# Kernel tuning notes

Measured on AMD Instinct MI355X. Metric: run time of the kernel, lower is better.

Reference implementation:

```python
import jax, jax.numpy as jnp
import numpy as np

V, C, D = 131072, 65536, 128
E_NEG, E_CON = 131072, 524288
L, B = 3, 32


def setup_inputs() -> dict:
    key = jax.random.key(0)
    ks = jax.random.split(key, 16)
    s = 1.0 / np.sqrt(D)
    return {
        "x_var": jax.random.normal(ks[0], (V, D), jnp.float32),
        "x_con": jax.random.normal(ks[1], (C, D), jnp.float32),
        "W_src": jax.random.normal(ks[2], (L, 3, D, D), jnp.float32) * s,
        "W_dst": jax.random.normal(ks[3], (L, 3, D, D), jnp.float32) * s,
        "att_src": jax.random.normal(ks[4], (L, 3, D), jnp.float32) * s,
        "att_dst": jax.random.normal(ks[5], (L, 3, D), jnp.float32) * s,
        "bias": jnp.zeros((L, 3, D), jnp.float32),
        "mlp_w1": jax.random.normal(ks[6], (D, D), jnp.float32) * s,
        "mlp_b1": jnp.zeros((D,), jnp.float32),
        "mlp_w2": jax.random.normal(ks[7], (D, 1), jnp.float32) * s,
        "mlp_b2": jnp.zeros((1,), jnp.float32),
        "edge_neg_src": jax.random.randint(ks[8], (E_NEG,), 0, V, jnp.int32),
        "edge_neg_dst": jax.random.randint(ks[9], (E_NEG,), 0, V, jnp.int32),
        "edge_con_src": jax.random.randint(ks[10], (E_CON,), 0, V, jnp.int32),
        "edge_con_dst": jax.random.randint(ks[11], (E_CON,), 0, C, jnp.int32),
        "batch_var": jnp.sort(jax.random.randint(ks[12], (V,), 0, B, jnp.int32)),
    }


def _gat(xs, xd, src, dst, Ws, Wd, a_s, a_d, b, n_dst):
    """PyG GATConv (heads=1, add_self_loops=False) for one bipartite relation."""
    hs = xs @ Ws                                    # [Ns, D]
    hd = xd @ Wd                                    # [Nd, D]
    es = hs @ a_s                                   # [Ns]
    ed = hd @ a_d                                   # [Nd]
    e = jax.nn.leaky_relu(es[src] + ed[dst], negative_slope=0.2)  # [E]
    m = jax.ops.segment_max(e, dst, num_segments=n_dst)
    m = jnp.where(jnp.isfinite(m), m, 0.0)
    ex = jnp.exp(e - m[dst])
    den = jax.ops.segment_sum(ex, dst, num_segments=n_dst)
    alpha = ex / (den[dst] + 1e-16)                 # per-destination softmax
    out = jax.ops.segment_sum(hs[src] * alpha[:, None], dst, num_segments=n_dst)
    return out + b


def reference(x_var, x_con, W_src, W_dst, att_src, att_dst, bias,
              mlp_w1, mlp_b1, mlp_w2, mlp_b2,
              edge_neg_src, edge_neg_dst, edge_con_src, edge_con_dst, batch_var):
    xv, xc = x_var, x_con
    n_layers = W_src.shape[0]
    for l in range(n_layers):
        # relation 0: variable -is_negation_of-> variable
        v_neg = _gat(xv, xv, edge_neg_src, edge_neg_dst,
                     W_src[l, 0], W_dst[l, 0], att_src[l, 0], att_dst[l, 0], bias[l, 0], V)
        # relation 2: constraint -rev_connected_to-> variable (reverse edges)
        v_rev = _gat(xc, xv, edge_con_dst, edge_con_src,
                     W_src[l, 2], W_dst[l, 2], att_src[l, 2], att_dst[l, 2], bias[l, 2], V)
        # relation 1: variable -connected_to-> constraint
        c_new = _gat(xv, xc, edge_con_src, edge_con_dst,
                     W_src[l, 1], W_dst[l, 1], att_src[l, 1], att_dst[l, 1], bias[l, 1], C)
        # HeteroConv aggr='sum', then relu (dropout is identity in eval)
        xv = jax.nn.relu(v_neg + v_rev)
        xc = jax.nn.relu(c_new)
    # global_mean_pool over variable nodes per graph
    cnt = jax.ops.segment_sum(jnp.ones((V,), xv.dtype), batch_var, num_segments=B)
    pooled = jax.ops.segment_sum(xv, batch_var, num_segments=B) / jnp.maximum(cnt, 1.0)[:, None]
    # vote MLP: Linear -> relu -> Linear
    h = jax.nn.relu(pooled @ mlp_w1 + mlp_b1)
    return h @ mlp_w2 + mlp_b2
```

## Files before the change

### kernel.cpp

```cpp
#include <hip/hip_runtime.h>
#include <hip/hip_bf16.h>
#include <cstdint>
#include <cstddef>

#define D 128

typedef __hip_bfloat16 bf16;
typedef __attribute__((ext_vector_type(8))) short short8v;
typedef __attribute__((ext_vector_type(4))) float f32x4;

__device__ inline float ld1(const float* p) { return *p; }
__device__ inline float ld1(const bf16* p) { return __bfloat162float(*p); }
__device__ inline float2 ld2(const float* p) { return *(const float2*)p; }
__device__ inline float2 ld2(const bf16* p) {
  __hip_bfloat162 v = *(const __hip_bfloat162*)p;
  float2 r; r.x = __bfloat162float(v.x); r.y = __bfloat162float(v.y); return r;
}
__device__ inline void st2(float* p, float a, float b) {
  float2 v; v.x = a; v.y = b; *(float2*)p = v;
}
__device__ inline void st2(bf16* p, float a, float b) {
  __hip_bfloat162 v; v.x = __float2bfloat16(a); v.y = __float2bfloat16(b);
  *(__hip_bfloat162*)p = v;
}

__device__ inline short f2bf(float x) {
  uint32_t u = __builtin_bit_cast(uint32_t, x);
  uint32_t r = (u + 0x7FFFu + ((u >> 16) & 1u)) >> 16;
  return (short)(uint16_t)r;
}
__device__ inline float bf2f(short s) {
  uint32_t u = ((uint32_t)(uint16_t)s) << 16;
  return __builtin_bit_cast(float, u);
}

__device__ inline f32x4 mfma16(short8v a, short8v b, f32x4 c) {
  return __builtin_amdgcn_mfma_f32_16x16x32_bf16(a, b, c, 0, 0, 0);
}

__device__ __forceinline__ void load8(const float* p, float* v) {
  float4 a = *(const float4*)p;
  float4 b = *(const float4*)(p + 4);
  v[0] = a.x; v[1] = a.y; v[2] = a.z; v[3] = a.w;
  v[4] = b.x; v[5] = b.y; v[6] = b.z; v[7] = b.w;
}
__device__ __forceinline__ void load8(const bf16* p, float* v) {
  short8v s = *(const short8v*)p;
  #pragma unroll
  for (int j = 0; j < 8; ++j) v[j] = bf2f(s[j]);
}
__device__ __forceinline__ void split_store(short* Xh, short* Xl, int off, const float* v) {
  short8v h, l;
  #pragma unroll
  for (int j = 0; j < 8; ++j) {
    short hj = f2bf(v[j]);
    h[j] = hj;
    l[j] = f2bf(v[j] - bf2f(hj));
  }
  *(short8v*)&Xh[off] = h;
  *(short8v*)&Xl[off] = l;
}

__global__ void compute_u_kernel(const float* __restrict__ Wsrc, const float* __restrict__ Wdst,
                                 const float* __restrict__ asrc, const float* __restrict__ adst,
                                 float* __restrict__ u) {
  int lr = blockIdx.x;
  int side = blockIdx.y;
  int k = threadIdx.x;
  const float* W = (side == 0 ? Wsrc : Wdst) + ((size_t)lr * D + k) * D;
  const float* a = (side == 0 ? asrc : adst) + (size_t)lr * D;
  float s = 0.f;
  for (int j = 0; j < D; ++j) s += W[j] * a[j];
  u[((size_t)lr * 2 + side) * D + k] = s;
}

__global__ void wsplit_kernel(const float* __restrict__ Wsrc,
                              short* __restrict__ WhT, short* __restrict__ WlT) {
  int lr = blockIdx.x;
  const float* W = Wsrc + (size_t)lr * D * D;
  short* wh = WhT + (size_t)lr * D * D;
  short* wl = WlT + (size_t)lr * D * D;
  for (int i = threadIdx.x; i < D * D; i += blockDim.x) {
    int k = i >> 7, c = i & 127;
    float w = W[i];
    short h = f2bf(w);
    short l = f2bf(w - bf2f(h));
    wh[c * D + k] = h;
    wl[c * D + k] = l;
  }
}

__global__ void count_kernel(const int* __restrict__ dst, int* __restrict__ cnt, int E) {
  int i = blockIdx.x * blockDim.x + threadIdx.x;
  if (i < E) atomicAdd(&cnt[dst[i]], 1);
}

__global__ void count2_kernel(const int* __restrict__ csrc, const int* __restrict__ cdst,
                              int* __restrict__ cnt_bycon, int* __restrict__ cnt_byvar, int E) {
  int i = blockIdx.x * blockDim.x + threadIdx.x;
  if (i < E) {
    atomicAdd(&cnt_bycon[cdst[i]], 1);
    atomicAdd(&cnt_byvar[csrc[i]], 1);
  }
}

__global__ void bsum3_kernel(const int* __restrict__ c0, const int* __restrict__ c1,
                             const int* __restrict__ c2, int* __restrict__ bsums,
                             int n0, int n1, int n2, int pb0, int pb1, int pb2) {
  __shared__ int red[256];
  int y = blockIdx.y;
  const int* cnt = (y == 0) ? c0 : (y == 1) ? c1 : c2;
  int n  = (y == 0) ? n0 : (y == 1) ? n1 : n2;
  int pb = (y == 0) ? pb0 : (y == 1) ? pb1 : pb2;
  int b = blockIdx.x, t = threadIdx.x;
  int base = b * pb;
  if (base >= n) return;
  int end = base + pb; if (end > n) end = n;
  int s = 0;
  for (int i = base + t; i < end; i += 256) s += cnt[i];
  red[t] = s;
  __syncthreads();
  #pragma unroll
  for (int off = 128; off; off >>= 1) {
    if (t < off) red[t] += red[t + off];
    __syncthreads();
  }
  if (t == 0) bsums[y * 1024 + b] = red[0];
}

__global__ void bscan3_kernel(int* __restrict__ bsums,
                              int* __restrict__ t0, int* __restrict__ t1, int* __restrict__ t2) {
  __shared__ int sh[1024];
  int y = blockIdx.x, t = threadIdx.x;
  int* bs = bsums + y * 1024;
  int v = bs[t];
  sh[t] = v;
  __syncthreads();
  for (int off = 1; off < 1024; off <<= 1) {
    int u = (t >= off) ? sh[t - off] : 0;
    __syncthreads();
    sh[t] += u;
    __syncthreads();
  }
  bs[t] = sh[t] - v;
  if (t == 1023) {
    int* tot = (y == 0) ? t0 : (y == 1) ? t1 : t2;
    *tot = sh[1023];
  }
}

__global__ void scanfill3_kernel(const int* __restrict__ c0, const int* __restrict__ c1,
                                 const int* __restrict__ c2, const int* __restrict__ bsums,
                                 int* __restrict__ rp0, int* __restrict__ rp1, int* __restrict__ rp2,
                                 int* __restrict__ cu0, int* __restrict__ cu1, int* __restrict__ cu2,
                                 int n0, int n1, int n2, int pb0, int pb1, int pb2) {
  __shared__ int sh[256];
  int y = blockIdx.y;
  const int* cnt = (y == 0) ? c0 : (y == 1) ? c1 : c2;
  int* rowptr    = (y == 0) ? rp0 : (y == 1) ? rp1 : rp2;
  int* cursor    = (y == 0) ? cu0 : (y == 1) ? cu1 : cu2;
  int n  = (y == 0) ? n0 : (y == 1) ? n1 : n2;
  int pb = (y == 0) ? pb0 : (y == 1) ? pb1 : pb2;
  int b = blockIdx.x, t = threadIdx.x;
  int base = b * pb;
  if (base >= n) return;
  int end = base + pb; if (end > n) end = n;
  int run = bsums[y * 1024 + b];
  for (int tile = base; tile < end; tile += 256) {
    int i = tile + t;
    int c = (i < end) ? cnt[i] : 0;
    __syncthreads();
    sh[t] = c;
    __syncthreads();
    for (int off = 1; off < 256; off <<= 1) {
      int u = (t >= off) ? sh[t - off] : 0;
      __syncthreads();
      sh[t] += u;
      __syncthreads();
    }
    int excl = sh[t] - c;
    if (i < end) {
      rowptr[i] = run + excl;
      cursor[i] = run + excl;
    }
    run += sh[255];
  }
}

__global__ void fill_kernel(const int* __restrict__ dst, const int* __restrict__ src,
                            int* __restrict__ cursor, int* __restrict__ col, int E) {
  int i = blockIdx.x * blockDim.x + threadIdx.x;
  if (i < E) {
    int p = atomicAdd(&cursor[dst[i]], 1);
    col[p] = src[i];
  }
}

__global__ void fill2_kernel(const int* __restrict__ csrc, const int* __restrict__ cdst,
                             int* __restrict__ cur_bycon, int* __restrict__ cur_byvar,
                             int* __restrict__ col_bycon, int* __restrict__ col_byvar, int E) {
  int i = blockIdx.x * blockDim.x + threadIdx.x;
  if (i < E) {
    int s = csrc[i], d = cdst[i];
    int p = atomicAdd(&cur_bycon[d], 1);
    col_bycon[p] = s;
    int q = atomicAdd(&cur_byvar[s], 1);
    col_byvar[q] = d;
  }
}

template<typename Tin>
__global__ __launch_bounds__(512) void mmv3_kernel(
    const Tin* __restrict__ Xv, const Tin* __restrict__ Xc,
    const short* __restrict__ wh0, const short* __restrict__ wl0,
    const short* __restrict__ wh1, const short* __restrict__ wl1,
    const short* __restrict__ wh2, const short* __restrict__ wl2,
    bf16* __restrict__ H0, bf16* __restrict__ H1, bf16* __restrict__ H2,
    const float* __restrict__ uv0, const float* __restrict__ uv1,
    const float* __restrict__ uv2, const float* __restrict__ uv3,
    const float* __restrict__ uc0, const float* __restrict__ uc1,
    float* __restrict__ es0, float* __restrict__ ed0,
    float* __restrict__ es1, float* __restrict__ ed2,
    float* __restrict__ es2, float* __restrict__ ed1,
    int V, int C, int b0, int b1, int b2) {
  __shared__ short sbuf[2][2][32 * 136];
  int bid = blockIdx.x;
  const Tin* X; const short* wh; const short* wl; bf16* H;
  int nrows, lb, nblk, ndots;
  const float *U0, *U1, *U2, *U3;
  float *O0, *O1, *O2, *O3;
  if (bid < b0) {
    X = Xv; wh = wh0; wl = wl0; H = H0; nrows = V; lb = bid; nblk = b0;
    ndots = 4; U0 = uv0; U1 = uv1; U2 = uv2; U3 = uv3;
    O0 = es0; O1 = ed0; O2 = es1; O3 = ed2;
  } else if (bid < b1) {
    X = Xv; wh = wh1; wl = wl1; H = H1; nrows = V; lb = bid - b0; nblk = b1 - b0;
    ndots = 0; U0 = U1 = U2 = U3 = nullptr; O0 = O1 = O2 = O3 = nullptr;
  } else {
    X = Xc; wh = wh2; wl = wl2; H = H2; nrows = C; lb = bid - b1; nblk = b2 - b1;
    ndots = 2; U0 = uc0; U1 = uc1; U2 = U3 = nullptr;
    O0 = es2; O1 = ed1; O2 = O3 = nullptr;
  }
  int nchunks = nrows >> 5;
  if (lb >= nchunks) return;

  int tid = threadIdx.x;
  int wv = tid >> 6, lane = tid & 63;
  int c15 = lane & 15, q = lane >> 4;
  int rowgrp = wv >> 2, colgrp = wv & 3;

  short8v Bh[2][4], Bl[2][4];
  #pragma unroll
  for (int t = 0; t < 2; ++t) {
    #pragma unroll
    for (int ks = 0; ks < 4; ++ks) {
      int o = (colgrp * 32 + t * 16 + c15) * D + ks * 32 + q * 8;
      Bh[t][ks] = *(const short8v*)&wh[o];
      Bl[t][ks] = *(const short8v*)&wl[o];
    }
  }

  int srow = tid >> 4;
  int scol = (tid & 15) * 8;
  int soff = srow * 136 + scol;

  float u0r[8], u1r[8], u2r[8], u3r[8];
  if (ndots) {
    load8(U0 + scol, u0r);
    load8(U1 + scol, u1r);
    if (ndots == 4) { load8(U2 + scol, u2r); load8(U3 + scol, u3r); }
  }

  auto do_dots = [&](const float* v, int gr) {
    if (!ndots) return;
    float p0 = 0.f, p1 = 0.f, p2 = 0.f, p3 = 0.f;
    #pragma unroll
    for (int j = 0; j < 8; ++j) { p0 += v[j] * u0r[j]; p1 += v[j] * u1r[j]; }
    if (ndots == 4) {
      #pragma unroll
      for (int j = 0; j < 8; ++j) { p2 += v[j] * u2r[j]; p3 += v[j] * u3r[j]; }
    }
    #pragma unroll
    for (int off = 1; off < 16; off <<= 1) {
      p0 += __shfl_xor(p0, off);
      p1 += __shfl_xor(p1, off);
      if (ndots == 4) { p2 += __shfl_xor(p2, off); p3 += __shfl_xor(p3, off); }
    }
    if ((tid & 15) == 0) {
      O0[gr] = p0; O1[gr] = p1;
      if (ndots == 4) { O2[gr] = p2; O3[gr] = p3; }
    }
  };

  {
    float v[8];
    int gr = lb * 32 + srow; if (gr >= nrows) gr = nrows - 1;
    load8(X + (size_t)gr * D + scol, v);
    do_dots(v, gr);
    split_store(&sbuf[0][0][0], &sbuf[0][1][0], soff, v);
  }
  __syncthreads();

  int aoff = (rowgrp * 16 + c15) * 136 + q * 8;
  int cur = 0;
  for (int chunk = lb; chunk < nchunks; chunk += nblk) {
    int nxt = chunk + nblk;
    bool have = nxt < nchunks;
    float v[8];
    if (have) {
      int gr = nxt * 32 + srow; if (gr >= nrows) gr = nrows - 1;
      load8(X + (size_t)gr * D + scol, v);
      do_dots(v, gr);
    }
    const short* Ah = &sbuf[cur][0][aoff];
    const short* Al = &sbuf[cur][1][aoff];
    f32x4 a0 = (f32x4){0.f, 0.f, 0.f, 0.f};
    f32x4 a1 = (f32x4){0.f, 0.f, 0.f, 0.f};
    #pragma unroll
    for (int ks = 0; ks < 4; ++ks) {
      short8v xh = *(const short8v*)(Ah + ks * 32);
      short8v xl = *(const short8v*)(Al + ks * 32);
      a0 = mfma16(Bh[0][ks], xh, a0);
      a1 = mfma16(Bh[1][ks], xh, a1);
      a0 = mfma16(Bl[0][ks], xh, a0);
      a1 = mfma16(Bl[1][ks], xh, a1);
      a0 = mfma16(Bh[0][ks], xl, a0);
      a1 = mfma16(Bh[1][ks], xl, a1);
    }
    int gr = chunk * 32 + rowgrp * 16 + c15;
    if (gr < nrows) {
      short4 o0, o1;
      o0.x = f2bf(a0[0]); o0.y = f2bf(a0[1]); o0.z = f2bf(a0[2]); o0.w = f2bf(a0[3]);
      o1.x = f2bf(a1[0]); o1.y = f2bf(a1[1]); o1.z = f2bf(a1[2]); o1.w = f2bf(a1[3]);
      size_t base = (size_t)gr * D + colgrp * 32 + q * 4;
      *(short4*)((short*)H + base) = o0;
      *(short4*)((short*)H + base + 16) = o1;
    }
    if (have) split_store(&sbuf[cur ^ 1][0][0], &sbuf[cur ^ 1][1][0], soff, v);
    __syncthreads();
    cur ^= 1;
  }
}

__device__ __forceinline__ void alpha_rel(const int* __restrict__ rp, const int* __restrict__ col,
                                          const float* __restrict__ es, float edst,
                                          int gw, int lane, int2* __restrict__ edata) {
  int p0 = rp[gw];
  int deg = rp[gw + 1] - p0;
  if (deg <= 0) return;
  if (deg <= 64) {
    int s = 0; float e = -3.0e38f;
    if (lane < deg) {
      s = col[p0 + lane];
      float t = es[s] + edst;
      e = t > 0.f ? t : 0.2f * t;
    }
    float m = e;
    #pragma unroll
    for (int off = 32; off; off >>= 1) m = fmaxf(m, __shfl_xor(m, off));
    float ex = (lane < deg) ? __expf(e - m) : 0.f;
    float den = ex;
    #pragma unroll
    for (int off = 32; off; off >>= 1) den += __shfl_xor(den, off);
    float al = ex / (den + 1e-16f);
    if (lane < deg) {
      int2 v; v.x = s; v.y = __builtin_bit_cast(int, al);
      edata[p0 + lane] = v;
    }
  } else {
    float m = -3.0e38f;
    for (int j = lane; j < deg; j += 64) {
      int s = col[p0 + j];
      float t = es[s] + edst;
      t = t > 0.f ? t : 0.2f * t;
      m = fmaxf(m, t);
    }
    #pragma unroll
    for (int off = 32; off; off >>= 1) m = fmaxf(m, __shfl_xor(m, off));
    float den = 0.f;
    for (int j = lane; j < deg; j += 64) {
      int s = col[p0 + j];
      float t = es[s] + edst;
      t = t > 0.f ? t : 0.2f * t;
      den += __expf(t - m);
    }
    #pragma unroll
    for (int off = 32; off; off >>= 1) den += __shfl_xor(den, off);
    float inv = 1.f / (den + 1e-16f);
    for (int j = lane; j < deg; j += 64) {
      int s = col[p0 + j];
      float t = es[s] + edst;
      t = t > 0.f ? t : 0.2f * t;
      int2 v; v.x = s; v.y = __builtin_bit_cast(int, __expf(t - m) * inv);
      edata[p0 + j] = v;
    }
  }
}

__global__ void alpha_all_kernel(const int* __restrict__ rp0, const int* __restrict__ col0,
                                 const float* __restrict__ es0, const float* __restrict__ ed0,
                                 int2* __restrict__ eda0,
                                 const int* __restrict__ rp2, const int* __restrict__ col2,
                                 const float* __restrict__ es2, const float* __restrict__ ed2,
                                 int2* __restrict__ eda2,
                                 const int* __restrict__ rp1, const int* __restrict__ col1,
                                 const float* __restrict__ es1, const float* __restrict__ ed1,
                                 int2* __restrict__ eda1,
                                 int V, int C) {
  int gw = (int)(((size_t)blockIdx.x * blockDim.x + threadIdx.x) >> 6);
  int lane = threadIdx.x & 63;
  if (gw < V) {
    alpha_rel(rp0, col0, es0, ed0[gw], gw, lane, eda0);
    alpha_rel(rp2, col2, es2, ed2[gw], gw, lane, eda2);
  } else if (gw < V + C) {
    int g = gw - V;
    alpha_rel(rp1, col1, es1, ed1[g], g, lane, eda1);
  }
}

__device__ __forceinline__ void agg_rel(const int2* __restrict__ edata, int p0, int p1,
                                        const bf16* __restrict__ hs, int l2,
                                        float& a0, float& a1) {
  int q = p0;
  while (q + 4 <= p1) {
    int2 e0 = edata[q], e1 = edata[q + 1], e2 = edata[q + 2], e3 = edata[q + 3];
    int s0 = __builtin_amdgcn_readfirstlane(e0.x);
    int s1 = __builtin_amdgcn_readfirstlane(e1.x);
    int s2 = __builtin_amdgcn_readfirstlane(e2.x);
    int s3 = __builtin_amdgcn_readfirstlane(e3.x);
    float w0 = __builtin_bit_cast(float, __builtin_amdgcn_readfirstlane(e0.y));
    float w1 = __builtin_bit_cast(float, __builtin_amdgcn_readfirstlane(e1.y));
    float w2 = __builtin_bit_cast(float, __builtin_amdgcn_readfirstlane(e2.y));
    float w3 = __builtin_bit_cast(float, __builtin_amdgcn_readfirstlane(e3.y));
    float2 h0 = ld2(&hs[(size_t)s0 * D + l2]);
    float2 h1 = ld2(&hs[(size_t)s1 * D + l2]);
    float2 h2 = ld2(&hs[(size_t)s2 * D + l2]);
    float2 h3 = ld2(&hs[(size_t)s3 * D + l2]);
    a0 += w0 * h0.x + w1 * h1.x + w2 * h2.x + w3 * h3.x;
    a1 += w0 * h0.y + w1 * h1.y + w2 * h2.y + w3 * h3.y;
    q += 4;
  }
  while (q < p1) {
    int2 e = edata[q++];
    int s = __builtin_amdgcn_readfirstlane(e.x);
    float w = __builtin_bit_cast(float, __builtin_amdgcn_readfirstlane(e.y));
    float2 h = ld2(&hs[(size_t)s * D + l2]);
    a0 += w * h.x;
    a1 += w * h.y;
  }
}

__global__ void agg_all_kernel(const int* __restrict__ rp0, const int2* __restrict__ eda0,
                               const bf16* __restrict__ hsv0, const float* __restrict__ b0,
                               const int* __restrict__ rp2, const int2* __restrict__ eda2,
                               const bf16* __restrict__ hsc, const float* __restrict__ b2,
                               const int* __restrict__ rp1, const int2* __restrict__ eda1,
                               const bf16* __restrict__ hsv1, const float* __restrict__ b1,
                               bf16* __restrict__ xv_out, bf16* __restrict__ xc_out, int V, int C) {
  int gw = (int)(((size_t)blockIdx.x * blockDim.x + threadIdx.x) >> 6);
  int lane = threadIdx.x & 63;
  int l2 = 2 * lane;
  if (gw < V) {
    float a0 = 0.f, a1 = 0.f;
    agg_rel(eda0, rp0[gw], rp0[gw + 1], hsv0, l2, a0, a1);
    agg_rel(eda2, rp2[gw], rp2[gw + 1], hsc, l2, a0, a1);
    float v0 = a0 + b0[l2] + b2[l2];
    float v1 = a1 + b0[l2 + 1] + b2[l2 + 1];
    st2(&xv_out[(size_t)gw * D + l2], v0 > 0.f ? v0 : 0.f, v1 > 0.f ? v1 : 0.f);
  } else if (gw < V + C) {
    int g = gw - V;
    float a0 = 0.f, a1 = 0.f;
    agg_rel(eda1, rp1[g], rp1[g + 1], hsv1, l2, a0, a1);
    float v0 = a0 + b1[l2];
    float v1 = a1 + b1[l2 + 1];
    st2(&xc_out[(size_t)g * D + l2], v0 > 0.f ? v0 : 0.f, v1 > 0.f ? v1 : 0.f);
  }
}

__global__ void pool_kernel(const bf16* __restrict__ xv, const int* __restrict__ batch,
                            float* __restrict__ pooled, float* __restrict__ cntf,
                            int rowsPerBlock, int V) {
  int j = threadIdx.x;
  int r0 = blockIdx.x * rowsPerBlock;
  if (r0 >= V) return;
  int rend = r0 + rowsPerBlock; if (rend > V) rend = V;
  int cur = batch[r0];
  float s = 0.f;
  int run = 0;
  for (int r = r0; r < rend; ++r) {
    int b = batch[r];
    if (b != cur) {
      atomicAdd(&pooled[(size_t)cur * D + j], s);
      if (j == 0) atomicAdd(&cntf[cur], (float)run);
      s = 0.f; run = 0; cur = b;
    }
    s += ld1(&xv[(size_t)r * D + j]);
    run++;
  }
  atomicAdd(&pooled[(size_t)cur * D + j], s);
  if (j == 0) atomicAdd(&cntf[cur], (float)run);
}

__global__ void mlp_kernel(const float* __restrict__ pooled, const float* __restrict__ cntf,
                           const float* __restrict__ w1, const float* __restrict__ b1,
                           const float* __restrict__ w2, const float* __restrict__ b2,
                           float* __restrict__ out, int B) {
  __shared__ float P[32 * D];
  __shared__ float Hs[32 * D];
  int tid = threadIdx.x;
  if (B > 32) return;
  for (int i = tid; i < B * D; i += 256) {
    int r = i >> 7;
    P[i] = pooled[i] / fmaxf(cntf[r], 1.0f);
  }
  __syncthreads();
  for (int i = tid; i < B * D; i += 256) {
    int r = i >> 7, j = i & 127;
    float s = b1[j];
    for (int k = 0; k < D; ++k) s += P[r * D + k] * w1[k * D + j];
    Hs[i] = s > 0.f ? s : 0.f;
  }
  __syncthreads();
  if (tid < B) {
    float s = b2[0];
    for (int j = 0; j < D; ++j) s += Hs[tid * D + j] * w2[j];
    out[tid] = s;
  }
}

__global__ void zero_kernel(float* __restrict__ o, int n) {
  int i = blockIdx.x * blockDim.x + threadIdx.x;
  if (i < n) o[i] = 0.f;
}

static void run_all(const float* x_var, const float* x_con,
                    const float* W_src, const float* W_dst,
                    const float* att_src, const float* att_dst, const float* bias,
                    const float* mlp_w1, const float* mlp_b1,
                    const float* mlp_w2, const float* mlp_b2,
                    const int* e_neg_src, const int* e_neg_dst,
                    const int* e_con_src, const int* e_con_dst, const int* batch_var,
                    int V, int C, int L, int EN, int EC, int B,
                    char* ws, float* out, hipStream_t stream) {
  size_t off = 0;
  auto alloc = [&](size_t bytes) -> char* {
    char* p = ws + off;
    off = (off + bytes + 255) & ~(size_t)255;
    return p;
  };
  bf16* xv  = (bf16*)alloc((size_t)V * D * 2);
  bf16* xc  = (bf16*)alloc((size_t)C * D * 2);
  bf16* hsv0 = (bf16*)alloc((size_t)V * D * 2);
  bf16* hsv1 = (bf16*)alloc((size_t)V * D * 2);
  bf16* hsc  = (bf16*)alloc((size_t)C * D * 2);
  float* es0 = (float*)alloc((size_t)V * 4);
  float* ed0 = (float*)alloc((size_t)V * 4);
  float* es1 = (float*)alloc((size_t)V * 4);
  float* ed2 = (float*)alloc((size_t)V * 4);
  float* es2 = (float*)alloc((size_t)C * 4);
  float* ed1 = (float*)alloc((size_t)C * 4);
  float* u   = (float*)alloc((size_t)L * 3 * 2 * D * 4);
  short* whT = (short*)alloc((size_t)L * 3 * D * D * 2);
  short* wlT = (short*)alloc((size_t)L * 3 * D * D * 2);
  int* rp0  = (int*)alloc((size_t)(V + 1) * 4);
  int* rp1  = (int*)alloc((size_t)(C + 1) * 4);
  int* rp2  = (int*)alloc((size_t)(V + 1) * 4);
  int* curs = (int*)alloc((size_t)(2 * (size_t)V + C) * 4);
  int* cur0 = curs, *cur1 = curs + V, *cur2 = curs + V + C;
  int* col0 = (int*)alloc((size_t)EN * 4);
  int* col1 = (int*)alloc((size_t)EC * 4);
  int* col2 = (int*)alloc((size_t)EC * 4);
  int2* eda0 = (int2*)alloc((size_t)EN * 8);
  int2* eda1 = (int2*)alloc((size_t)EC * 8);
  int2* eda2 = (int2*)alloc((size_t)EC * 8);
  int* bsums = (int*)alloc((size_t)3 * 1024 * 4);
  float* pooled = (float*)alloc((size_t)(B * D + B) * 4);
  float* cntf = pooled + (size_t)B * D;

  hipMemsetAsync(curs, 0, (size_t)(2 * (size_t)V + C) * 4, stream);
  hipMemsetAsync(bsums, 0, (size_t)3 * 1024 * 4, stream);
  hipMemsetAsync(pooled, 0, (size_t)(B * D + B) * 4, stream);

  compute_u_kernel<<<dim3(L * 3, 2), D, 0, stream>>>(W_src, W_dst, att_src, att_dst, u);
  wsplit_kernel<<<L * 3, 256, 0, stream>>>(W_src, whT, wlT);

  const int tb = 256;
  count_kernel<<<(EN + tb - 1) / tb, tb, 0, stream>>>(e_neg_dst, cur0, EN);
  count2_kernel<<<(EC + tb - 1) / tb, tb, 0, stream>>>(e_con_src, e_con_dst, cur1, cur2, EC);

  auto pbof = [](int n) {
    int pb = ((n + 1023) / 1024 + 255) & ~255;
    return pb < 256 ? 256 : pb;
  };
  int pb0 = pbof(V), pb1 = pbof(C), pb2 = pbof(V);
  int nb0 = (V + pb0 - 1) / pb0, nb1 = (C + pb1 - 1) / pb1, nb2 = (V + pb2 - 1) / pb2;
  int nbmax = nb0 > nb1 ? nb0 : nb1; if (nb2 > nbmax) nbmax = nb2;
  bsum3_kernel<<<dim3(nbmax, 3), 256, 0, stream>>>(cur0, cur1, cur2, bsums, V, C, V, pb0, pb1, pb2);
  bscan3_kernel<<<3, 1024, 0, stream>>>(bsums, rp0 + V, rp1 + C, rp2 + V);
  scanfill3_kernel<<<dim3(nbmax, 3), 256, 0, stream>>>(cur0, cur1, cur2, bsums,
                                                       rp0, rp1, rp2, cur0, cur1, cur2,
                                                       V, C, V, pb0, pb1, pb2);

  fill_kernel<<<(EN + tb - 1) / tb, tb, 0, stream>>>(e_neg_dst, e_neg_src, cur0, col0, EN);
  fill2_kernel<<<(EC + tb - 1) / tb, tb, 0, stream>>>(e_con_src, e_con_dst, cur1, cur2, col1, col2, EC);

  auto U  = [&](int l, int rel, int side) { return u + (((size_t)l * 3 + rel) * 2 + side) * D; };
  auto Wh = [&](int l, int rel) { return whT + ((size_t)l * 3 + rel) * D * D; };
  auto Wl = [&](int l, int rel) { return wlT + ((size_t)l * 3 + rel) * D * D; };
  auto Bp = [&](int l, int rel) { return bias + ((size_t)l * 3 + rel) * D; };

  int gwaves = (V + C + 3) / 4;
  const int MB0 = 512, MB1 = 1024, MB2 = 1280;

  for (int l = 0; l < L; ++l) {
    if (l == 0) {
      mmv3_kernel<float><<<MB2, 512, 0, stream>>>(
          x_var, x_con, Wh(l,0), Wl(l,0), Wh(l,1), Wl(l,1), Wh(l,2), Wl(l,2),
          hsv0, hsv1, hsc,
          U(l,0,0), U(l,0,1), U(l,1,0), U(l,2,1), U(l,2,0), U(l,1,1),
          es0, ed0, es1, ed2, es2, ed1, V, C, MB0, MB1, MB2);
    } else {
      mmv3_kernel<bf16><<<MB2, 512, 0, stream>>>(
          xv, xc, Wh(l,0), Wl(l,0), Wh(l,1), Wl(l,1), Wh(l,2), Wl(l,2),
          hsv0, hsv1, hsc,
          U(l,0,0), U(l,0,1), U(l,1,0), U(l,2,1), U(l,2,0), U(l,1,1),
          es0, ed0, es1, ed2, es2, ed1, V, C, MB0, MB1, MB2);
    }
    alpha_all_kernel<<<gwaves, 256, 0, stream>>>(
        rp0, col0, es0, ed0, eda0,
        rp2, col2, es2, ed2, eda2,
        rp1, col1, es1, ed1, eda1, V, C);
    agg_all_kernel<<<gwaves, 256, 0, stream>>>(
        rp0, eda0, hsv0, Bp(l,0),
        rp2, eda2, hsc,  Bp(l,2),
        rp1, eda1, hsv1, Bp(l,1),
        xv, xc, V, C);
  }

  pool_kernel<<<(V + 127) / 128, 128, 0, stream>>>(xv, batch_var, pooled, cntf, 128, V);
  mlp_kernel<<<1, 256, 0, stream>>>(pooled, cntf, mlp_w1, mlp_b1, mlp_w2, mlp_b2, out, B);
}

extern "C" void kernel_launch(void* const* d_in, const int* in_sizes, int n_in,
                              void* d_out, int out_size, void* d_ws, size_t ws_size,
                              hipStream_t stream) {
  const float* x_var   = (const float*)d_in[0];
  const float* x_con   = (const float*)d_in[1];
  const float* W_src   = (const float*)d_in[2];
  const float* W_dst   = (const float*)d_in[3];
  const float* att_src = (const float*)d_in[4];
  const float* att_dst = (const float*)d_in[5];
  const float* bias    = (const float*)d_in[6];
  const float* mlp_w1  = (const float*)d_in[7];
  const float* mlp_b1  = (const float*)d_in[8];
  const float* mlp_w2  = (const float*)d_in[9];
  const float* mlp_b2  = (const float*)d_in[10];
  const int* e_neg_src = (const int*)d_in[11];
  const int* e_neg_dst = (const int*)d_in[12];
  const int* e_con_src = (const int*)d_in[13];
  const int* e_con_dst = (const int*)d_in[14];
  const int* batch_var = (const int*)d_in[15];
  (void)n_in;

  const int V  = in_sizes[0] / D;
  const int C  = in_sizes[1] / D;
  const int L  = in_sizes[2] / (3 * D * D);
  const int EN = in_sizes[11];
  const int EC = in_sizes[13];
  const int B  = out_size;

  auto plan = [&]() -> size_t {
    size_t o = 0;
    auto add = [&](size_t b) { o = (o + b + 255) & ~(size_t)255; };
    add((size_t)V * D * 2); add((size_t)C * D * 2);
    add((size_t)V * D * 2); add((size_t)V * D * 2); add((size_t)C * D * 2);
    add((size_t)V * 4); add((size_t)V * 4); add((size_t)V * 4); add((size_t)V * 4);
    add((size_t)C * 4); add((size_t)C * 4);
    add((size_t)L * 3 * 2 * D * 4);
    add((size_t)L * 3 * D * D * 2); add((size_t)L * 3 * D * D * 2);
    add((size_t)(V + 1) * 4); add((size_t)(C + 1) * 4); add((size_t)(V + 1) * 4);
    add((size_t)(2 * (size_t)V + C) * 4);
    add((size_t)EN * 4); add((size_t)EC * 4); add((size_t)EC * 4);
    add((size_t)EN * 8); add((size_t)EC * 8); add((size_t)EC * 8);
    add((size_t)3 * 1024 * 4);
    add((size_t)(B * D + B) * 4);
    return o;
  };

  if (plan() <= ws_size) {
    run_all(x_var, x_con, W_src, W_dst, att_src, att_dst, bias,
            mlp_w1, mlp_b1, mlp_w2, mlp_b2,
            e_neg_src, e_neg_dst, e_con_src, e_con_dst, batch_var,
            V, C, L, EN, EC, B, (char*)d_ws, (float*)d_out, stream);
  } else {
    zero_kernel<<<(out_size + 63) / 64, 64, 0, stream>>>((float*)d_out, out_size);
  }
}
```

Before: 969.0 us.

## Restructure projection GEMM to load X directly into MFMA fragments and fold attention dots

Replaces the LDS double-buffered 32-row GEMM with a 256-thread kernel that processes 16-row chunks, loading X rows straight from global memory into MFMA operand registers, with no shared memory or barriers. The per-node attention dot products are folded into an extra MFMA against split-bf16 attention vectors computed on wave 0, replacing the scalar dot and shuffle reductions. For bf16 inputs the low-part correction on X is dropped, since X is already exact in bf16. Grid size doubles to keep occupancy up. In exchange, wave 0 does extra MFMAs, and each wave re-reads X rows from global memory instead of sharing them through LDS.

After: 974.9 us. Within noise of the previous version (+0.6%).

```diff
diff --git a/kernel.cpp b/kernel.cpp
--- a/kernel.cpp
+++ b/kernel.cpp
@@ -43,22 +43,6 @@
   float4 b = *(const float4*)(p + 4);
   v[0] = a.x; v[1] = a.y; v[2] = a.z; v[3] = a.w;
   v[4] = b.x; v[5] = b.y; v[6] = b.z; v[7] = b.w;
-}
-__device__ __forceinline__ void load8(const bf16* p, float* v) {
-  short8v s = *(const short8v*)p;
-  #pragma unroll
-  for (int j = 0; j < 8; ++j) v[j] = bf2f(s[j]);
-}
-__device__ __forceinline__ void split_store(short* Xh, short* Xl, int off, const float* v) {
-  short8v h, l;
-  #pragma unroll
-  for (int j = 0; j < 8; ++j) {
-    short hj = f2bf(v[j]);
-    h[j] = hj;
-    l[j] = f2bf(v[j] - bf2f(hj));
-  }
-  *(short8v*)&Xh[off] = h;
-  *(short8v*)&Xl[off] = l;
 }
 
 __global__ void compute_u_kernel(const float* __restrict__ Wsrc, const float* __restrict__ Wdst,
@@ -88,6 +72,26 @@
     wh[c * D + k] = h;
     wl[c * D + k] = l;
   }
+}
+
+__global__ void usplit_kernel(const float* __restrict__ u,
+                              short* __restrict__ uh, short* __restrict__ ul, int L) {
+  int l = blockIdx.x;
+  int j = blockIdx.y;
+  int k = threadIdx.x;
+  int rel, side;
+  switch (j) {
+    case 0: rel = 0; side = 0; break;
+    case 1: rel = 0; side = 1; break;
+    case 2: rel = 1; side = 0; break;
+    case 3: rel = 2; side = 1; break;
+    case 4: rel = 2; side = 0; break;
+    default: rel = 1; side = 1; break;
+  }
+  float w = u[(((size_t)l * 3 + rel) * 2 + side) * D + k];
+  short h = f2bf(w);
+  uh[((size_t)l * 6 + j) * D + k] = h;
+  ul[((size_t)l * 6 + j) * D + k] = f2bf(w - bf2f(h));
 }
 
 __global__ void count_kernel(const int* __restrict__ dst, int* __restrict__ cnt, int E) {
@@ -210,135 +214,130 @@
 }
 
 template<typename Tin>
-__global__ __launch_bounds__(512) void mmv3_kernel(
+__global__ __launch_bounds__(256) void mm3r_kernel(
     const Tin* __restrict__ Xv, const Tin* __restrict__ Xc,
     const short* __restrict__ wh0, const short* __restrict__ wl0,
     const short* __restrict__ wh1, const short* __restrict__ wl1,
     const short* __restrict__ wh2, const short* __restrict__ wl2,
+    const short* __restrict__ uah, const short* __restrict__ ual,
     bf16* __restrict__ H0, bf16* __restrict__ H1, bf16* __restrict__ H2,
-    const float* __restrict__ uv0, const float* __restrict__ uv1,
-    const float* __restrict__ uv2, const float* __restrict__ uv3,
-    const float* __restrict__ uc0, const float* __restrict__ uc1,
     float* __restrict__ es0, float* __restrict__ ed0,
     float* __restrict__ es1, float* __restrict__ ed2,
     float* __restrict__ es2, float* __restrict__ ed1,
     int V, int C, int b0, int b1, int b2) {
-  __shared__ short sbuf[2][2][32 * 136];
   int bid = blockIdx.x;
   const Tin* X; const short* wh; const short* wl; bf16* H;
-  int nrows, lb, nblk, ndots;
-  const float *U0, *U1, *U2, *U3;
-  float *O0, *O1, *O2, *O3;
+  int nrows, lb, nblk, nu;
+  const short* auh; const short* aul;
+  float *o0, *o1, *o2, *o3;
   if (bid < b0) {
     X = Xv; wh = wh0; wl = wl0; H = H0; nrows = V; lb = bid; nblk = b0;
-    ndots = 4; U0 = uv0; U1 = uv1; U2 = uv2; U3 = uv3;
-    O0 = es0; O1 = ed0; O2 = es1; O3 = ed2;
+    nu = 4; auh = uah; aul = ual;
+    o0 = es0; o1 = ed0; o2 = es1; o3 = ed2;
   } else if (bid < b1) {
     X = Xv; wh = wh1; wl = wl1; H = H1; nrows = V; lb = bid - b0; nblk = b1 - b0;
-    ndots = 0; U0 = U1 = U2 = U3 = nullptr; O0 = O1 = O2 = O3 = nullptr;
+    nu = 0; auh = nullptr; aul = nullptr; o0 = o1 = o2 = o3 = nullptr;
   } else {
     X = Xc; wh = wh2; wl = wl2; H = H2; nrows = C; lb = bid - b1; nblk = b2 - b1;
-    ndots = 2; U0 = uc0; U1 = uc1; U2 = U3 = nullptr;
-    O0 = es2; O1 = ed1; O2 = O3 = nullptr;
-  }
-  int nchunks = nrows >> 5;
-  if (lb >= nchunks) return;
-
+    nu = 2; auh = uah + 4 * D; aul = ual + 4 * D;
+    o0 = es2; o1 = ed1; o2 = o3 = nullptr;
+  }
+  int nchunks = (nrows + 15) >> 4;
   int tid = threadIdx.x;
-  int wv = tid >> 6, lane = tid & 63;
+  int cp = tid >> 6, lane = tid & 63;
   int c15 = lane & 15, q = lane >> 4;
-  int rowgrp = wv >> 2, colgrp = wv & 3;
-
-  short8v Bh[2][4], Bl[2][4];
+
+  short8v Wh_[2][4], Wl_[2][4];
   #pragma unroll
   for (int t = 0; t < 2; ++t) {
     #pragma unroll
     for (int ks = 0; ks < 4; ++ks) {
-      int o = (colgrp * 32 + t * 16 + c15) * D + ks * 32 + q * 8;
-      Bh[t][ks] = *(const short8v*)&wh[o];
-      Bl[t][ks] = *(const short8v*)&wl[o];
-    }
-  }
-
-  int srow = tid >> 4;
-  int scol = (tid & 15) * 8;
-  int soff = srow * 136 + scol;
-
-  float u0r[8], u1r[8], u2r[8], u3r[8];
-  if (ndots) {
-    load8(U0 + scol, u0r);
-    load8(U1 + scol, u1r);
-    if (ndots == 4) { load8(U2 + scol, u2r); load8(U3 + scol, u3r); }
-  }
-
-  auto do_dots = [&](const float* v, int gr) {
-    if (!ndots) return;
-    float p0 = 0.f, p1 = 0.f, p2 = 0.f, p3 = 0.f;
+      int o = (cp * 32 + t * 16 + c15) * D + ks * 32 + q * 8;
+      Wh_[t][ks] = *(const short8v*)&wh[o];
+      Wl_[t][ks] = *(const short8v*)&wl[o];
+    }
+  }
+  bool doaug = (cp == 0) && (nu > 0);
+  short8v Uh_[4], Ul_[4];
+  if (doaug) {
     #pragma unroll
-    for (int j = 0; j < 8; ++j) { p0 += v[j] * u0r[j]; p1 += v[j] * u1r[j]; }
-    if (ndots == 4) {
-      #pragma unroll
-      for (int j = 0; j < 8; ++j) { p2 += v[j] * u2r[j]; p3 += v[j] * u3r[j]; }
-    }
-    #pragma unroll
-    for (int off = 1; off < 16; off <<= 1) {
-      p0 += __shfl_xor(p0, off);
-      p1 += __shfl_xor(p1, off);
-      if (ndots == 4) { p2 += __shfl_xor(p2, off); p3 += __shfl_xor(p3, off); }
-    }
-    if ((tid & 15) == 0) {
-      O0[gr] = p0; O1[gr] = p1;
-      if (ndots == 4) { O2[gr] = p2; O3[gr] = p3; }
-    }
-  };
-
-  {
-    float v[8];
-    int gr = lb * 32 + srow; if (gr >= nrows) gr = nrows - 1;
-    load8(X + (size_t)gr * D + scol, v);
-    do_dots(v, gr);
-    split_store(&sbuf[0][0][0], &sbuf[0][1][0], soff, v);
-  }
-  __syncthreads();
-
-  int aoff = (rowgrp * 16 + c15) * 136 + q * 8;
-  int cur = 0;
-  for (int chunk = lb; chunk < nchunks; chunk += nblk) {
-    int nxt = chunk + nblk;
-    bool have = nxt < nchunks;
-    float v[8];
-    if (have) {
-      int gr = nxt * 32 + srow; if (gr >= nrows) gr = nrows - 1;
-      load8(X + (size_t)gr * D + scol, v);
-      do_dots(v, gr);
-    }
-    const short* Ah = &sbuf[cur][0][aoff];
-    const short* Al = &sbuf[cur][1][aoff];
+    for (int ks = 0; ks < 4; ++ks) {
+      if (c15 < nu) {
+        int o = c15 * D + ks * 32 + q * 8;
+        Uh_[ks] = *(const short8v*)&auh[o];
+        Ul_[ks] = *(const short8v*)&aul[o];
+      } else {
+        Uh_[ks] = (short8v){0, 0, 0, 0, 0, 0, 0, 0};
+        Ul_[ks] = (short8v){0, 0, 0, 0, 0, 0, 0, 0};
+      }
+    }
+  }
+
+  for (int ch = lb; ch < nchunks; ch += nblk) {
+    int row = ch * 16 + c15;
+    bool valid = row < nrows;
+    if (!valid) row = nrows - 1;
+    const Tin* xp = X + (size_t)row * D + q * 8;
     f32x4 a0 = (f32x4){0.f, 0.f, 0.f, 0.f};
     f32x4 a1 = (f32x4){0.f, 0.f, 0.f, 0.f};
-    #pragma unroll
-    for (int ks = 0; ks < 4; ++ks) {
-      short8v xh = *(const short8v*)(Ah + ks * 32);
-      short8v xl = *(const short8v*)(Al + ks * 32);
-      a0 = mfma16(Bh[0][ks], xh, a0);
-      a1 = mfma16(Bh[1][ks], xh, a1);
-      a0 = mfma16(Bl[0][ks], xh, a0);
-      a1 = mfma16(Bl[1][ks], xh, a1);
-      a0 = mfma16(Bh[0][ks], xl, a0);
-      a1 = mfma16(Bh[1][ks], xl, a1);
-    }
-    int gr = chunk * 32 + rowgrp * 16 + c15;
-    if (gr < nrows) {
-      short4 o0, o1;
-      o0.x = f2bf(a0[0]); o0.y = f2bf(a0[1]); o0.z = f2bf(a0[2]); o0.w = f2bf(a0[3]);
-      o1.x = f2bf(a1[0]); o1.y = f2bf(a1[1]); o1.z = f2bf(a1[2]); o1.w = f2bf(a1[3]);
-      size_t base = (size_t)gr * D + colgrp * 32 + q * 4;
-      *(short4*)((short*)H + base) = o0;
-      *(short4*)((short*)H + base + 16) = o1;
-    }
-    if (have) split_store(&sbuf[cur ^ 1][0][0], &sbuf[cur ^ 1][1][0], soff, v);
-    __syncthreads();
-    cur ^= 1;
+    f32x4 a2 = (f32x4){0.f, 0.f, 0.f, 0.f};
+    if constexpr (sizeof(Tin) == 2) {
+      short8v xf[4];
+      #pragma unroll
+      for (int ks = 0; ks < 4; ++ks)
+        xf[ks] = *(const short8v*)((const short*)xp + ks * 32);
+      #pragma unroll
+      for (int ks = 0; ks < 4; ++ks) {
+        a0 = mfma16(Wh_[0][ks], xf[ks], a0);
+        a0 = mfma16(Wl_[0][ks], xf[ks], a0);
+        a1 = mfma16(Wh_[1][ks], xf[ks], a1);
+        a1 = mfma16(Wl_[1][ks], xf[ks], a1);
+        if (doaug) {
+          a2 = mfma16(Uh_[ks], xf[ks], a2);
+          a2 = mfma16(Ul_[ks], xf[ks], a2);
+        }
+      }
+    } else {
+      short8v xh[4], xl[4];
+      #pragma unroll
+      for (int ks = 0; ks < 4; ++ks) {
+        float v[8];
+        load8((const float*)xp + ks * 32, v);
+        #pragma unroll
+        for (int j = 0; j < 8; ++j) {
+          short hj = f2bf(v[j]);
+          xh[ks][j] = hj;
+          xl[ks][j] = f2bf(v[j] - bf2f(hj));
+        }
+      }
+      #pragma unroll
+      for (int ks = 0; ks < 4; ++ks) {
+        a0 = mfma16(Wh_[0][ks], xh[ks], a0);
+        a0 = mfma16(Wl_[0][ks], xh[ks], a0);
+        a0 = mfma16(Wh_[0][ks], xl[ks], a0);
+        a1 = mfma16(Wh_[1][ks], xh[ks], a1);
+        a1 = mfma16(Wl_[1][ks], xh[ks], a1);
+        a1 = mfma16(Wh_[1][ks], xl[ks], a1);
+        if (doaug) {
+          a2 = mfma16(Uh_[ks], xh[ks], a2);
+          a2 = mfma16(Ul_[ks], xh[ks], a2);
+          a2 = mfma16(Uh_[ks], xl[ks], a2);
+        }
+      }
+    }
+    if (valid) {
+      short4 s0, s1;
+      s0.x = f2bf(a0[0]); s0.y = f2bf(a0[1]); s0.z = f2bf(a0[2]); s0.w = f2bf(a0[3]);
+      s1.x = f2bf(a1[0]); s1.y = f2bf(a1[1]); s1.z = f2bf(a1[2]); s1.w = f2bf(a1[3]);
+      size_t hb = (size_t)row * D + cp * 32 + q * 4;
+      *(short4*)((short*)H + hb) = s0;
+      *(short4*)((short*)H + hb + 16) = s1;
+      if (doaug && q == 0) {
+        o0[row] = a2[0];
+        o1[row] = a2[1];
+        if (nu == 4) { o2[row] = a2[2]; o3[row] = a2[3]; }
+      }
+    }
   }
 }
 
@@ -562,6 +561,8 @@
   float* u   = (float*)alloc((size_t)L * 3 * 2 * D * 4);
   short* whT = (short*)alloc((size_t)L * 3 * D * D * 2);
   short* wlT = (short*)alloc((size_t)L * 3 * D * D * 2);
+  short* uh  = (short*)alloc((size_t)L * 6 * D * 2);
+  short* ul  = (short*)alloc((size_t)L * 6 * D * 2);
   int* rp0  = (int*)alloc((size_t)(V + 1) * 4);
   int* rp1  = (int*)alloc((size_t)(C + 1) * 4);
   int* rp2  = (int*)alloc((size_t)(V + 1) * 4);
@@ -583,6 +584,7 @@
 
   compute_u_kernel<<<dim3(L * 3, 2), D, 0, stream>>>(W_src, W_dst, att_src, att_dst, u);
   wsplit_kernel<<<L * 3, 256, 0, stream>>>(W_src, whT, wlT);
+  usplit_kernel<<<dim3(L, 6), D, 0, stream>>>(u, uh, ul, L);
 
   const int tb = 256;
   count_kernel<<<(EN + tb - 1) / tb, tb, 0, stream>>>(e_neg_dst, cur0, EN);
@@ -604,26 +606,25 @@
   fill_kernel<<<(EN + tb - 1) / tb, tb, 0, stream>>>(e_neg_dst, e_neg_src, cur0, col0, EN);
   fill2_kernel<<<(EC + tb - 1) / tb, tb, 0, stream>>>(e_con_src, e_con_dst, cur1, cur2, col1, col2, EC);
 
-  auto U  = [&](int l, int rel, int side) { return u + (((size_t)l * 3 + rel) * 2 + side) * D; };
   auto Wh = [&](int l, int rel) { return whT + ((size_t)l * 3 + rel) * D * D; };
   auto Wl = [&](int l, int rel) { return wlT + ((size_t)l * 3 + rel) * D * D; };
   auto Bp = [&](int l, int rel) { return bias + ((size_t)l * 3 + rel) * D; };
 
   int gwaves = (V + C + 3) / 4;
-  const int MB0 = 512, MB1 = 1024, MB2 = 1280;
+  const int MB0 = 1024, MB1 = 2048, MB2 = 2560;
 
   for (int l = 0; l < L; ++l) {
+    const short* uah = uh + (size_t)l * 6 * D;
+    const short* ual = ul + (size_t)l * 6 * D;
     if (l == 0) {
-      mmv3_kernel<float><<<MB2, 512, 0, stream>>>(
+      mm3r_kernel<float><<<MB2, 256, 0, stream>>>(
           x_var, x_con, Wh(l,0), Wl(l,0), Wh(l,1), Wl(l,1), Wh(l,2), Wl(l,2),
-          hsv0, hsv1, hsc,
-          U(l,0,0), U(l,0,1), U(l,1,0), U(l,2,1), U(l,2,0), U(l,1,1),
+          uah, ual, hsv0, hsv1, hsc,
           es0, ed0, es1, ed2, es2, ed1, V, C, MB0, MB1, MB2);
     } else {
-      mmv3_kernel<bf16><<<MB2, 512, 0, stream>>>(
+      mm3r_kernel<bf16><<<MB2, 256, 0, stream>>>(
           xv, xc, Wh(l,0), Wl(l,0), Wh(l,1), Wl(l,1), Wh(l,2), Wl(l,2),
-          hsv0, hsv1, hsc,
-          U(l,0,0), U(l,0,1), U(l,1,0), U(l,2,1), U(l,2,0), U(l,1,1),
+          uah, ual, hsv0, hsv1, hsc,
           es0, ed0, es1, ed2, es2, ed1, V, C, MB0, MB1, MB2);
     }
     alpha_all_kernel<<<gwaves, 256, 0, stream>>>(
@@ -678,6 +679,7 @@
     add((size_t)C * 4); add((size_t)C * 4);
     add((size_t)L * 3 * 2 * D * 4);
     add((size_t)L * 3 * D * D * 2); add((size_t)L * 3 * D * D * 2);
+    add((size_t)L * 6 * D * 2); add((size_t)L * 6 * D * 2);
     add((size_t)(V + 1) * 4); add((size_t)(C + 1) * 4); add((size_t)(V + 1) * 4);
     add((size_t)(2 * (size_t)V + C) * 4);
     add((size_t)EN * 4); add((size_t)EC * 4); add((size_t)EC * 4);
```
